# Kernel tuning notes

Hardware: AMD Instinct MI355X
Metric: run time of the kernel (lower is better)

## Reference

```python
import jax, jax.numpy as jnp
import numpy as np

B, S, D, H = 4, 2048, 512, 8
DK = D // H
SCALE = 1.0 / np.sqrt(DK)


def setup_inputs() -> dict:
    key = jax.random.key(0)
    kx, kq, kk, kv = jax.random.split(key, 4)
    w_std = np.sqrt(2.0 / (D + D))  # xavier-ish scale
    return {
        "x": jax.random.normal(kx, (B, S, D), dtype=jnp.float32),
        "W_Q": jax.random.normal(kq, (D, D), dtype=jnp.float32) * w_std,
        "W_K": jax.random.normal(kk, (D, D), dtype=jnp.float32) * w_std,
        "W_V": jax.random.normal(kv, (D, D), dtype=jnp.float32) * w_std,
    }


def reference(x, W_Q, W_K, W_V):
    # torch Linear(bias=False): y = x @ W.T
    q = jnp.einsum('bsd,ed->bse', x, W_Q).reshape(B, S, H, DK).transpose(0, 2, 1, 3)
    k = jnp.einsum('bsd,ed->bse', x, W_K).reshape(B, S, H, DK).transpose(0, 2, 1, 3)
    v = jnp.einsum('bsd,ed->bse', x, W_V).reshape(B, S, H, DK).transpose(0, 2, 1, 3)
    scores = jnp.einsum('bhqd,bhkd->bhqk', q, k) * SCALE  # [B,H,S,S]
    scores_exp = jnp.exp(scores)  # faithful: no max-subtraction in original
    attn = scores_exp / (scores_exp.sum(axis=-1, keepdims=True) + 1e-8)
    context = jnp.einsum('bhqk,bhkd->bhqd', attn, v)
    return context.transpose(0, 2, 1, 3).reshape(B, S, D)
```

## Files before the change

kernel.cpp:

```cpp
#include <hip/hip_runtime.h>
#include <hip/hip_bf16.h>

#define Bsz 4
#define Ssz 2048
#define Dsz 512
#define Hsz 8
#define DKsz 64

typedef __bf16 bf16x8 __attribute__((ext_vector_type(8)));
typedef __bf16 bf16x4 __attribute__((ext_vector_type(4)));
typedef float f32x4 __attribute__((ext_vector_type(4)));

#define SWE(c, row) ((((c) ^ ((row) & 7)) * 8))

#define GLL16(g, l) __builtin_amdgcn_global_load_lds(                      \
    (const __attribute__((address_space(1))) void*)(g),                    \
    (__attribute__((address_space(3))) void*)(l), 16, 0, 0)

__global__ __launch_bounds__(256) void cvt_kernel(
    const float* __restrict__ x, const float* __restrict__ Wq,
    const float* __restrict__ Wk, const float* __restrict__ Wv,
    __bf16* __restrict__ xb, __bf16* __restrict__ Wb)
{
    const int i = blockIdx.x * 256 + threadIdx.x;
    const int XN4 = (Bsz * Ssz * Dsz) / 4;
    const float* src;
    __bf16* dst;
    int off;
    if (i < XN4) {
        src = x; dst = xb; off = i;
    } else {
        int j = i - XN4;
        int w = j >> 16;
        off = j & 65535;
        src = (w == 0) ? Wq : (w == 1) ? Wk : Wv;
        dst = Wb + (size_t)w * (Dsz * Dsz);
    }
    float4 v = ((const float4*)src)[off];
    __bf16 o[4] = {(__bf16)v.x, (__bf16)v.y, (__bf16)v.z, (__bf16)v.w};
    *(uint2*)(dst + (size_t)off * 4) = *(uint2*)o;
}

__global__ __launch_bounds__(256, 3) void qkv_kernel(
    const __bf16* __restrict__ xb, const __bf16* __restrict__ Wb,
    __bf16* __restrict__ Qo, __bf16* __restrict__ Ko, __bf16* __restrict__ Vo)
{
    __shared__ __bf16 xs[128][64];
    __shared__ __bf16 wsh[128][64];

    const int tid  = threadIdx.x;
    const int lane = tid & 63;
    const int wave = tid >> 6;
    const int quad = lane >> 4;
    const int l16  = lane & 15;
    const int wm   = (wave & 1) * 64;
    const int wn   = (wave >> 1) * 64;

    const int lin = blockIdx.x;
    const int xcd = lin & 7;
    const int idx = lin >> 3;
    const int tnw = idx % 12;
    const int tmh = idx / 12;
    const int tm  = (tmh * 8 + xcd) * 128;
    const int tn  = (tnw & 3) * 128;
    const int which = tnw >> 2;
    const bool VM = (which == 2);
    const __bf16* W = Wb + (size_t)which * (Dsz * Dsz);

    const int rl  = lane >> 3;
    const int gch = (lane & 7) ^ rl;
    const __bf16* xsrc = xb + (size_t)(tm + wave * 8 + rl) * Dsz + gch * 8;
    const __bf16* wsrc = W  + (size_t)(tn + wave * 8 + rl) * Dsz + gch * 8;

    f32x4 acc[4][4];
    #pragma unroll
    for (int i = 0; i < 4; ++i)
        #pragma unroll
        for (int j = 0; j < 4; ++j) acc[i][j] = (f32x4){0.f, 0.f, 0.f, 0.f};

    const __bf16 (*Ash)[64] = VM ? xs : wsh;
    const __bf16 (*Bsh)[64] = VM ? wsh : xs;

    for (int k0 = 0; k0 < Dsz; k0 += 64) {
        __syncthreads();
        #pragma unroll
        for (int i = 0; i < 4; ++i) {
            GLL16(xsrc + (size_t)(32 * i) * Dsz + k0, &xs[wave * 8 + 32 * i][0]);
            GLL16(wsrc + (size_t)(32 * i) * Dsz + k0, &wsh[wave * 8 + 32 * i][0]);
        }
        asm volatile("s_waitcnt vmcnt(0)" ::: "memory");
        __syncthreads();

        #pragma unroll
        for (int kk = 0; kk < 2; ++kk) {
            bf16x8 fa[4], fb[4];
            #pragma unroll
            for (int mi = 0; mi < 4; ++mi) {
                const int row = wm + mi * 16 + l16;
                fa[mi] = *(const bf16x8*)&Ash[row][SWE(kk * 4 + quad, row)];
            }
            #pragma unroll
            for (int ni = 0; ni < 4; ++ni) {
                const int row = wn + ni * 16 + l16;
                fb[ni] = *(const bf16x8*)&Bsh[row][SWE(kk * 4 + quad, row)];
            }
            #pragma unroll
            for (int mi = 0; mi < 4; ++mi)
                #pragma unroll
                for (int ni = 0; ni < 4; ++ni)
                    acc[mi][ni] = __builtin_amdgcn_mfma_f32_16x16x32_bf16(
                        fa[mi], fb[ni], acc[mi][ni], 0, 0, 0);
        }
    }

    if (!VM) {
        const float scale = (which == 0) ? 0.125f * 1.44269504088896340736f : 1.0f;
        __bf16* dst = (which == 0) ? Qo : Ko;
        #pragma unroll
        for (int mi = 0; mi < 4; ++mi) {
            const int e0 = tn + wm + mi * 16 + quad * 4;
            const int h = e0 >> 6, d0 = e0 & 63;
            #pragma unroll
            for (int ni = 0; ni < 4; ++ni) {
                const int sf = tm + wn + ni * 16 + l16;
                const int b = sf >> 11, s = sf & (Ssz - 1);
                bf16x4 p;
                #pragma unroll
                for (int r = 0; r < 4; ++r) p[r] = (__bf16)(acc[mi][ni][r] * scale);
                *(bf16x4*)&dst[((((size_t)(b * Hsz + h) * Ssz + s)) << 6) + d0] = p;
            }
        }
    } else {
        #pragma unroll
        for (int mi = 0; mi < 4; ++mi) {
            const int sf0 = tm + wm + mi * 16 + quad * 4;
            const int b = sf0 >> 11, s0 = sf0 & (Ssz - 1);
            #pragma unroll
            for (int ni = 0; ni < 4; ++ni) {
                const int e = tn + wn + ni * 16 + l16;
                const int h = e >> 6, d = e & 63;
                bf16x4 p;
                #pragma unroll
                for (int r = 0; r < 4; ++r) p[r] = (__bf16)acc[mi][ni][r];
                *(bf16x4*)&Vo[(((size_t)(b * Hsz + h) * DKsz + d) << 11) + s0] = p;
            }
        }
    }
}

__global__ __launch_bounds__(256, 2) void attn_kernel(
    const __bf16* __restrict__ Q, const __bf16* __restrict__ K,
    const __bf16* __restrict__ VT, float* __restrict__ out)
{
    __shared__ __bf16 ks[64][64];
    __shared__ __bf16 vs[64][64];
    __shared__ __bf16 ps[4][16][64];

    const int tid  = threadIdx.x;
    const int lane = tid & 63;
    const int wave = tid >> 6;
    const int quad = lane >> 4;
    const int l16  = lane & 15;

    const int bh = blockIdx.x;
    const int qt = blockIdx.y;
    const int b  = bh >> 3;
    const int h  = bh & 7;

    const __bf16* Qb = Q  + (size_t)bh * Ssz * DKsz;
    const __bf16* Kb = K  + (size_t)bh * Ssz * DKsz;
    const __bf16* Vb = VT + (size_t)bh * DKsz * Ssz;

    bf16x8 qf[2][2];
    #pragma unroll
    for (int qs = 0; qs < 2; ++qs) {
        const __bf16* qrow = Qb + (size_t)(qt * 128 + wave * 32 + qs * 16 + l16) * DKsz;
        qf[qs][0] = *(const bf16x8*)(qrow + quad * 8);
        qf[qs][1] = *(const bf16x8*)(qrow + 32 + quad * 8);
    }

    bf16x8 ones;
    #pragma unroll
    for (int i = 0; i < 8; ++i) ones[i] = (__bf16)1.0f;

    f32x4 oacc[2][4];
    #pragma unroll
    for (int qs = 0; qs < 2; ++qs)
        #pragma unroll
        for (int i = 0; i < 4; ++i) oacc[qs][i] = (f32x4){0.f, 0.f, 0.f, 0.f};
    f32x4 lacc[2] = {(f32x4){0.f, 0.f, 0.f, 0.f}, (f32x4){0.f, 0.f, 0.f, 0.f}};

    const int srow = tid >> 3;
    const int sc   = tid & 7;
    const int swz  = SWE(sc, srow);

    const __bf16* kg = Kb + (size_t)srow * DKsz + sc * 8;
    const __bf16* vg = Vb + (size_t)srow * Ssz + sc * 8;

    bf16x8 pk0 = *(const bf16x8*)(kg);
    bf16x8 pk1 = *(const bf16x8*)(kg + (size_t)32 * DKsz);
    bf16x8 pv0 = *(const bf16x8*)(vg);
    bf16x8 pv1 = *(const bf16x8*)(vg + (size_t)32 * Ssz);

    for (int kb = 0; kb < Ssz; kb += 64) {
        __syncthreads();
        *(bf16x8*)&ks[srow][swz]      = pk0;
        *(bf16x8*)&ks[srow + 32][swz] = pk1;
        *(bf16x8*)&vs[srow][swz]      = pv0;
        *(bf16x8*)&vs[srow + 32][swz] = pv1;
        __syncthreads();

        if (kb + 64 < Ssz) {
            pk0 = *(const bf16x8*)(kg + (size_t)(kb + 64) * DKsz);
            pk1 = *(const bf16x8*)(kg + (size_t)(kb + 96) * DKsz);
            pv0 = *(const bf16x8*)(vg + kb + 64);
            pv1 = *(const bf16x8*)(vg + (size_t)32 * Ssz + kb + 64);
        }

        bf16x8 kf[2][4], vf[2][4];
        #pragma unroll
        for (int kk = 0; kk < 2; ++kk)
            #pragma unroll
            for (int ns = 0; ns < 4; ++ns) {
                const int row = ns * 16 + l16;
                kf[kk][ns] = *(const bf16x8*)&ks[row][SWE(kk * 4 + quad, row)];
                vf[kk][ns] = *(const bf16x8*)&vs[row][SWE(kk * 4 + quad, row)];
            }

        #pragma unroll
        for (int qs = 0; qs < 2; ++qs) {
            __builtin_amdgcn_s_setprio(1);
            f32x4 st[4];
            #pragma unroll
            for (int ns = 0; ns < 4; ++ns) {
                f32x4 t = (f32x4){0.f, 0.f, 0.f, 0.f};
                t = __builtin_amdgcn_mfma_f32_16x16x32_bf16(kf[0][ns], qf[qs][0], t, 0, 0, 0);
                t = __builtin_amdgcn_mfma_f32_16x16x32_bf16(kf[1][ns], qf[qs][1], t, 0, 0, 0);
                st[ns] = t;
            }
            __builtin_amdgcn_s_setprio(0);

            #pragma unroll
            for (int ns = 0; ns < 4; ++ns) {
                bf16x4 pp;
                #pragma unroll
                for (int r = 0; r < 4; ++r)
                    pp[r] = (__bf16)__builtin_amdgcn_exp2f(st[ns][r]);
                const int c = ns * 2 + (quad >> 1);
                *(bf16x4*)&ps[wave][l16][((c ^ (l16 & 7)) << 3) + ((quad & 1) << 2)] = pp;
            }
            const bf16x8 af0 = *(const bf16x8*)&ps[wave][l16][SWE(quad, l16)];
            const bf16x8 af1 = *(const bf16x8*)&ps[wave][l16][SWE(4 + quad, l16)];

            __builtin_amdgcn_s_setprio(1);
            #pragma unroll
            for (int ns = 0; ns < 4; ++ns) {
                oacc[qs][ns] = __builtin_amdgcn_mfma_f32_16x16x32_bf16(vf[0][ns], af0, oacc[qs][ns], 0, 0, 0);
                oacc[qs][ns] = __builtin_amdgcn_mfma_f32_16x16x32_bf16(vf[1][ns], af1, oacc[qs][ns], 0, 0, 0);
            }
            lacc[qs] = __builtin_amdgcn_mfma_f32_16x16x32_bf16(ones, af0, lacc[qs], 0, 0, 0);
            lacc[qs] = __builtin_amdgcn_mfma_f32_16x16x32_bf16(ones, af1, lacc[qs], 0, 0, 0);
            __builtin_amdgcn_s_setprio(0);
        }
    }

    #pragma unroll
    for (int qs = 0; qs < 2; ++qs) {
        const float linv = 1.f / (lacc[qs][0] + 1e-8f);
        const int q = qt * 128 + wave * 32 + qs * 16 + l16;
        float* obase = out + ((size_t)b * Ssz + q) * Dsz + h * DKsz;
        #pragma unroll
        for (int ns = 0; ns < 4; ++ns) {
            f32x4 o = oacc[qs][ns] * linv;
            *(f32x4*)(obase + ns * 16 + quad * 4) = o;
        }
    }
}

extern "C" void kernel_launch(void* const* d_in, const int* in_sizes, int n_in,
                              void* d_out, int out_size, void* d_ws, size_t ws_size,
                              hipStream_t stream) {
    const float* x  = (const float*)d_in[0];
    const float* Wq = (const float*)d_in[1];
    const float* Wk = (const float*)d_in[2];
    const float* Wv = (const float*)d_in[3];
    float* out = (float*)d_out;

    const size_t per = (size_t)Bsz * Hsz * Ssz * DKsz;
    __bf16* Qw  = (__bf16*)d_ws;
    __bf16* Kw  = Qw + per;
    __bf16* VTw = Kw + per;
    __bf16* xb  = VTw + per;
    __bf16* Wb  = xb + per;

    cvt_kernel<<<4864, 256, 0, stream>>>(x, Wq, Wk, Wv, xb, Wb);
    qkv_kernel<<<768, 256, 0, stream>>>(xb, Wb, Qw, Kw, VTw);
    attn_kernel<<<dim3(Bsz * Hsz, Ssz / 128), 256, 0, stream>>>(Qw, Kw, VTw, out);
}
```

Measured before the change: 134.4 us.

## Double-buffer K/V tiles in LDS via direct global-to-LDS loads

Replaces the register-staged K/V prefetch with global_load_lds DMA into a double-buffered LDS tile, so the next tile streams in while the current one is computed, with one barrier per tile instead of two. It also batches QK^T for both query sub-tiles before the exp/PV phase, using separate P scratch buffers to raise MFMA independence. The cost is doubled LDS for K/V plus an extra P buffer, which may lower occupancy. It also relies on a lane-XOR source swizzle matching the LDS read swizzle.

Result: slower. 139.8 us (+4.0%).

```diff
diff --git a/kernel.cpp b/kernel.cpp
--- a/kernel.cpp
+++ b/kernel.cpp
@@ -152,9 +152,10 @@
     const __bf16* __restrict__ Q, const __bf16* __restrict__ K,
     const __bf16* __restrict__ VT, float* __restrict__ out)
 {
-    __shared__ __bf16 ks[64][64];
-    __shared__ __bf16 vs[64][64];
-    __shared__ __bf16 ps[4][16][64];
+    __shared__ __bf16 ks[2][64][64];
+    __shared__ __bf16 vs[2][64][64];
+    __shared__ __bf16 psA[4][16][64];
+    __shared__ __bf16 psB[4][16][64];
 
     const int tid  = threadIdx.x;
     const int lane = tid & 63;
@@ -190,78 +191,91 @@
         for (int i = 0; i < 4; ++i) oacc[qs][i] = (f32x4){0.f, 0.f, 0.f, 0.f};
     f32x4 lacc[2] = {(f32x4){0.f, 0.f, 0.f, 0.f}, (f32x4){0.f, 0.f, 0.f, 0.f}};
 
-    const int srow = tid >> 3;
-    const int sc   = tid & 7;
-    const int swz  = SWE(sc, srow);
-
-    const __bf16* kg = Kb + (size_t)srow * DKsz + sc * 8;
-    const __bf16* vg = Vb + (size_t)srow * Ssz + sc * 8;
-
-    bf16x8 pk0 = *(const bf16x8*)(kg);
-    bf16x8 pk1 = *(const bf16x8*)(kg + (size_t)32 * DKsz);
-    bf16x8 pv0 = *(const bf16x8*)(vg);
-    bf16x8 pv1 = *(const bf16x8*)(vg + (size_t)32 * Ssz);
-
-    for (int kb = 0; kb < Ssz; kb += 64) {
-        __syncthreads();
-        *(bf16x8*)&ks[srow][swz]      = pk0;
-        *(bf16x8*)&ks[srow + 32][swz] = pk1;
-        *(bf16x8*)&vs[srow][swz]      = pv0;
-        *(bf16x8*)&vs[srow + 32][swz] = pv1;
-        __syncthreads();
-
-        if (kb + 64 < Ssz) {
-            pk0 = *(const bf16x8*)(kg + (size_t)(kb + 64) * DKsz);
-            pk1 = *(const bf16x8*)(kg + (size_t)(kb + 96) * DKsz);
-            pv0 = *(const bf16x8*)(vg + kb + 64);
-            pv1 = *(const bf16x8*)(vg + (size_t)32 * Ssz + kb + 64);
-        }
-
-        bf16x8 kf[2][4], vf[2][4];
-        #pragma unroll
-        for (int kk = 0; kk < 2; ++kk)
-            #pragma unroll
-            for (int ns = 0; ns < 4; ++ns) {
-                const int row = ns * 16 + l16;
-                kf[kk][ns] = *(const bf16x8*)&ks[row][SWE(kk * 4 + quad, row)];
-                vf[kk][ns] = *(const bf16x8*)&vs[row][SWE(kk * 4 + quad, row)];
-            }
-
-        #pragma unroll
-        for (int qs = 0; qs < 2; ++qs) {
-            __builtin_amdgcn_s_setprio(1);
-            f32x4 st[4];
-            #pragma unroll
-            for (int ns = 0; ns < 4; ++ns) {
-                f32x4 t = (f32x4){0.f, 0.f, 0.f, 0.f};
-                t = __builtin_amdgcn_mfma_f32_16x16x32_bf16(kf[0][ns], qf[qs][0], t, 0, 0, 0);
-                t = __builtin_amdgcn_mfma_f32_16x16x32_bf16(kf[1][ns], qf[qs][1], t, 0, 0, 0);
-                st[ns] = t;
-            }
-            __builtin_amdgcn_s_setprio(0);
-
-            #pragma unroll
-            for (int ns = 0; ns < 4; ++ns) {
-                bf16x4 pp;
-                #pragma unroll
-                for (int r = 0; r < 4; ++r)
-                    pp[r] = (__bf16)__builtin_amdgcn_exp2f(st[ns][r]);
-                const int c = ns * 2 + (quad >> 1);
-                *(bf16x4*)&ps[wave][l16][((c ^ (l16 & 7)) << 3) + ((quad & 1) << 2)] = pp;
-            }
-            const bf16x8 af0 = *(const bf16x8*)&ps[wave][l16][SWE(quad, l16)];
-            const bf16x8 af1 = *(const bf16x8*)&ps[wave][l16][SWE(4 + quad, l16)];
-
-            __builtin_amdgcn_s_setprio(1);
-            #pragma unroll
-            for (int ns = 0; ns < 4; ++ns) {
-                oacc[qs][ns] = __builtin_amdgcn_mfma_f32_16x16x32_bf16(vf[0][ns], af0, oacc[qs][ns], 0, 0, 0);
-                oacc[qs][ns] = __builtin_amdgcn_mfma_f32_16x16x32_bf16(vf[1][ns], af1, oacc[qs][ns], 0, 0, 0);
-            }
-            lacc[qs] = __builtin_amdgcn_mfma_f32_16x16x32_bf16(ones, af0, lacc[qs], 0, 0, 0);
-            lacc[qs] = __builtin_amdgcn_mfma_f32_16x16x32_bf16(ones, af1, lacc[qs], 0, 0, 0);
-            __builtin_amdgcn_s_setprio(0);
-        }
+    const int rl  = lane >> 3;
+    const int gch = (lane & 7) ^ rl;
+
+#define STAGE_KV(DST, KBASE)                                                   \
+    do {                                                                       \
+        const __bf16* kgs = Kb + (size_t)((KBASE) + wave * 8 + rl) * DKsz      \
+                               + gch * 8;                                      \
+        const __bf16* vgs = Vb + (size_t)(wave * 8 + rl) * Ssz + (KBASE)       \
+                               + gch * 8;                                      \
+        GLL16(kgs,                        &ks[DST][wave * 8][0]);              \
+        GLL16(kgs + (size_t)32 * DKsz,    &ks[DST][wave * 8 + 32][0]);         \
+        GLL16(vgs,                        &vs[DST][wave * 8][0]);              \
+        GLL16(vgs + (size_t)32 * Ssz,     &vs[DST][wave * 8 + 32][0]);         \
+    } while (0)
+
+    STAGE_KV(0, 0);
+    asm volatile("s_waitcnt vmcnt(0)\n\ts_barrier" ::: "memory");
+
+#define ATTN_TILE(CUR, KB)                                                     \
+    do {                                                                       \
+        if ((KB) + 64 < Ssz) STAGE_KV((CUR) ^ 1, (KB) + 64);                   \
+        bf16x8 kf[2][4], vf[2][4];                                             \
+        _Pragma("unroll")                                                      \
+        for (int kk = 0; kk < 2; ++kk)                                         \
+            _Pragma("unroll")                                                  \
+            for (int ns = 0; ns < 4; ++ns) {                                   \
+                const int row = ns * 16 + l16;                                 \
+                kf[kk][ns] = *(const bf16x8*)&ks[CUR][row][SWE(kk*4+quad,row)];\
+                vf[kk][ns] = *(const bf16x8*)&vs[CUR][row][SWE(kk*4+quad,row)];\
+            }                                                                  \
+        __builtin_amdgcn_s_setprio(1);                                         \
+        f32x4 st[2][4];                                                        \
+        _Pragma("unroll")                                                      \
+        for (int qs = 0; qs < 2; ++qs)                                         \
+            _Pragma("unroll")                                                  \
+            for (int ns = 0; ns < 4; ++ns) {                                   \
+                f32x4 t = (f32x4){0.f, 0.f, 0.f, 0.f};                         \
+                t = __builtin_amdgcn_mfma_f32_16x16x32_bf16(                   \
+                        kf[0][ns], qf[qs][0], t, 0, 0, 0);                     \
+                t = __builtin_amdgcn_mfma_f32_16x16x32_bf16(                   \
+                        kf[1][ns], qf[qs][1], t, 0, 0, 0);                     \
+                st[qs][ns] = t;                                                \
+            }                                                                  \
+        __builtin_amdgcn_s_setprio(0);                                         \
+        _Pragma("unroll")                                                      \
+        for (int qs = 0; qs < 2; ++qs)                                         \
+            _Pragma("unroll")                                                  \
+            for (int ns = 0; ns < 4; ++ns) {                                   \
+                bf16x4 pp;                                                     \
+                _Pragma("unroll")                                              \
+                for (int r = 0; r < 4; ++r)                                    \
+                    pp[r] = (__bf16)__builtin_amdgcn_exp2f(st[qs][ns][r]);     \
+                __bf16* pbase = qs ? &psB[wave][l16][0] : &psA[wave][l16][0];  \
+                const int c = ns * 2 + (quad >> 1);                            \
+                *(bf16x4*)&pbase[((c ^ (l16 & 7)) << 3) + ((quad & 1) << 2)]   \
+                    = pp;                                                      \
+            }                                                                  \
+        bf16x8 af[2][2];                                                       \
+        af[0][0] = *(const bf16x8*)&psA[wave][l16][SWE(quad, l16)];            \
+        af[0][1] = *(const bf16x8*)&psA[wave][l16][SWE(4 + quad, l16)];        \
+        af[1][0] = *(const bf16x8*)&psB[wave][l16][SWE(quad, l16)];            \
+        af[1][1] = *(const bf16x8*)&psB[wave][l16][SWE(4 + quad, l16)];        \
+        __builtin_amdgcn_s_setprio(1);                                         \
+        _Pragma("unroll")                                                      \
+        for (int qs = 0; qs < 2; ++qs) {                                       \
+            _Pragma("unroll")                                                  \
+            for (int ns = 0; ns < 4; ++ns) {                                   \
+                oacc[qs][ns] = __builtin_amdgcn_mfma_f32_16x16x32_bf16(        \
+                    vf[0][ns], af[qs][0], oacc[qs][ns], 0, 0, 0);              \
+                oacc[qs][ns] = __builtin_amdgcn_mfma_f32_16x16x32_bf16(        \
+                    vf[1][ns], af[qs][1], oacc[qs][ns], 0, 0, 0);              \
+            }                                                                  \
+            lacc[qs] = __builtin_amdgcn_mfma_f32_16x16x32_bf16(                \
+                ones, af[qs][0], lacc[qs], 0, 0, 0);                           \
+            lacc[qs] = __builtin_amdgcn_mfma_f32_16x16x32_bf16(                \
+                ones, af[qs][1], lacc[qs], 0, 0, 0);                           \
+        }                                                                      \
+        __builtin_amdgcn_s_setprio(0);                                         \
+        asm volatile("s_waitcnt vmcnt(0) lgkmcnt(0)\n\ts_barrier"              \
+                     ::: "memory");                                           \
+    } while (0)
+
+    for (int kb = 0; kb < Ssz; kb += 128) {
+        ATTN_TILE(0, kb);
+        ATTN_TILE(1, kb + 64);
     }
 
     #pragma unroll
@@ -275,6 +289,8 @@
             *(f32x4*)(obase + ns * 16 + quad * 4) = o;
         }
     }
+#undef ATTN_TILE
+#undef STAGE_KV
 }
 
 extern "C" void kernel_launch(void* const* d_in, const int* in_sizes, int n_in,
```
